# Optimization experiments

Hardware: AMD Instinct MI355X
Metric: run time of the kernel (lower is better)

## Reference

```python
import jax, jax.numpy as jnp
import numpy as np

B, T, C = 32, 2048, 1024  # batch, seq_len (<= block_size), n_embd
HEAD_SIZE = 128


def setup_inputs() -> dict:
    key = jax.random.key(0)
    kx, kk, kq, kv = jax.random.split(key, 4)
    std = 0.02  # CustomLinear init: normal(0, 0.02)
    return {
        "x": jax.random.normal(kx, (B, T, C), dtype=jnp.float32),
        "Wk": jax.random.normal(kk, (HEAD_SIZE, C), dtype=jnp.float32) * std,
        "Wq": jax.random.normal(kq, (HEAD_SIZE, C), dtype=jnp.float32) * std,
        "Wv": jax.random.normal(kv, (HEAD_SIZE, C), dtype=jnp.float32) * std,
    }


def reference(x, Wk, Wq, Wv):
    # x: [B, T, C]; W*: [head_size, C] (torch Linear layout, no bias)
    Bb, Tt, Cc = x.shape
    k = jnp.einsum("btc,hc->bth", x, Wk)
    q = jnp.einsum("btc,hc->bth", x, Wq)
    v = jnp.einsum("btc,hc->bth", x, Wv)
    # NOTE: original scales by C**-0.5 (n_embd), not head_size**-0.5
    wei = jnp.einsum("bth,bsh->bts", q, k) * (Cc ** -0.5)
    causal = jnp.tril(jnp.ones((Tt, Tt), dtype=bool))  # tril[:T,:T]
    wei = jnp.where(causal, wei, -jnp.inf)
    wei = jax.nn.softmax(wei, axis=-1)
    return jnp.einsum("bts,bsh->bth", wei, v)  # [B, T, head_size]
```

## Files before the change

### kernel.cpp

```cpp
#include <hip/hip_runtime.h>
#include <hip/hip_bf16.h>

typedef __bf16 bf8_t __attribute__((ext_vector_type(8)));
typedef __bf16 bf4_t __attribute__((ext_vector_type(4)));
typedef float f4_t __attribute__((ext_vector_type(4)));

#define B_ 32
#define T_ 2048
#define C_ 1024
#define H_ 128

__global__ __launch_bounds__(256, 2) void proj_kernel(
    const float* __restrict__ x,
    const float* __restrict__ Wk, const float* __restrict__ Wq, const float* __restrict__ Wv,
    __bf16* __restrict__ Kb, __bf16* __restrict__ Qb, __bf16* __restrict__ VtG)
{
    __shared__ __bf16 Xs[64][72];
    __shared__ __bf16 Ws[384][72];

    const int m0   = blockIdx.x * 64;
    const int tid  = threadIdx.x;
    const int lane = tid & 63;
    const int wid  = tid >> 6;
    const int lr   = lane & 15;
    const int quad = lane >> 4;

    f4_t acc[3][4][2];
    #pragma unroll
    for (int s = 0; s < 3; s++)
        for (int mi = 0; mi < 4; mi++)
            for (int ni = 0; ni < 2; ni++) acc[s][mi][ni] = f4_t{0.f, 0.f, 0.f, 0.f};

    const int srow = tid >> 4;
    const int sc4  = (tid & 15) << 2;

    float4 xr[4];
    #pragma unroll
    for (int i = 0; i < 4; i++)
        xr[i] = *(const float4*)(x + (size_t)(m0 + srow + i * 16) * C_ + sc4);

    for (int kkI = 0; kkI < 16; kkI++) {
        const int kk = kkI * 64;
        __syncthreads();
        #pragma unroll
        for (int i = 0; i < 4; i++) {
            float4 f = xr[i];
            *(bf4_t*)&Xs[srow + i * 16][sc4] =
                bf4_t{(__bf16)f.x, (__bf16)f.y, (__bf16)f.z, (__bf16)f.w};
        }
        #pragma unroll
        for (int i = 0; i < 24; i++) {
            const int row = srow + i * 16;
            const float* Wp = (row < 128) ? Wk : (row < 256) ? Wq : Wv;
            float4 f = *(const float4*)(Wp + (size_t)(row & 127) * C_ + kk + sc4);
            *(bf4_t*)&Ws[row][sc4] =
                bf4_t{(__bf16)f.x, (__bf16)f.y, (__bf16)f.z, (__bf16)f.w};
        }
        __syncthreads();
        if (kkI < 15) {
            #pragma unroll
            for (int i = 0; i < 4; i++)
                xr[i] = *(const float4*)(x + (size_t)(m0 + srow + i * 16) * C_ + kk + 64 + sc4);
        }
        #pragma unroll
        for (int ks = 0; ks < 2; ks++) {
            const int kb = ks * 32 + quad * 8;
            bf8_t xa[4];
            #pragma unroll
            for (int mi = 0; mi < 4; mi++) xa[mi] = *(const bf8_t*)&Xs[mi * 16 + lr][kb];
            #pragma unroll
            for (int sel = 0; sel < 3; sel++) {
                bf8_t wb[2];
                #pragma unroll
                for (int ni = 0; ni < 2; ni++)
                    wb[ni] = *(const bf8_t*)&Ws[sel * 128 + wid * 32 + ni * 16 + lr][kb];
                if (sel < 2) {
                    #pragma unroll
                    for (int mi = 0; mi < 4; mi++)
                        for (int ni = 0; ni < 2; ni++)
                            acc[sel][mi][ni] = __builtin_amdgcn_mfma_f32_16x16x32_bf16(
                                xa[mi], wb[ni], acc[sel][mi][ni], 0, 0, 0);
                } else {
                    #pragma unroll
                    for (int mi = 0; mi < 4; mi++)
                        for (int ni = 0; ni < 2; ni++)
                            acc[2][mi][ni] = __builtin_amdgcn_mfma_f32_16x16x32_bf16(
                                wb[ni], xa[mi], acc[2][mi][ni], 0, 0, 0);
                }
            }
        }
    }

    #pragma unroll
    for (int sel = 0; sel < 2; sel++) {
        __bf16* Out = (sel == 0) ? Kb : Qb;
        #pragma unroll
        for (int mi = 0; mi < 4; mi++)
            for (int ni = 0; ni < 2; ni++) {
                const int col = wid * 32 + ni * 16 + lr;
                #pragma unroll
                for (int r = 0; r < 4; r++) {
                    const int row = m0 + mi * 16 + quad * 4 + r;
                    Out[(size_t)row * H_ + col] = (__bf16)acc[sel][mi][ni][r];
                }
            }
    }
    {
        const int bb = m0 >> 11;
        const int t0 = m0 & (T_ - 1);
        #pragma unroll
        for (int mi = 0; mi < 4; mi++)
            for (int ni = 0; ni < 2; ni++) {
                const int tok = t0 + mi * 16 + lr;
                #pragma unroll
                for (int r = 0; r < 4; r++) {
                    const int h = wid * 32 + ni * 16 + quad * 4 + r;
                    VtG[(size_t)bb * H_ * T_ + (size_t)h * T_ + tok] = (__bf16)acc[2][mi][ni][r];
                }
            }
    }
}

__global__ __launch_bounds__(512, 4) void flash_kernel(
    const __bf16* __restrict__ Qb, const __bf16* __restrict__ Kb,
    const __bf16* __restrict__ VtG, float* __restrict__ Out)
{
    __shared__ __bf16 Ks[64][136];
    __shared__ __bf16 Vt[128][72];
    __shared__ __bf16 Ps[128][72];

    const int qt = 15 - blockIdx.x;
    const int b  = blockIdx.y;
    const size_t kqbase = (size_t)b * T_ * H_;
    const size_t vbase  = (size_t)b * H_ * T_;

    const int tid  = threadIdx.x;
    const int lane = tid & 63;
    const int w    = tid >> 6;
    const int lr   = lane & 15;
    const int quad = lane >> 4;

    bf8_t qf[4];
    {
        const __bf16* qp = Qb + kqbase + (size_t)(qt * 128 + w * 16 + lr) * H_ + quad * 8;
        #pragma unroll
        for (int ks = 0; ks < 4; ks++) qf[ks] = *(const bf8_t*)(qp + ks * 32);
    }

    f4_t o[8];
    #pragma unroll
    for (int n = 0; n < 8; n++) o[n] = f4_t{0.f, 0.f, 0.f, 0.f};
    float ls[4] = {0.f, 0.f, 0.f, 0.f};

    const float sc = 0.03125f * 1.4426950408889634f;
    const int jmax = 2 * qt + 1;

    for (int j = 0; j <= jmax; j++) {
        __syncthreads();
        #pragma unroll
        for (int i = 0; i < 2; i++) {
            const int u = tid + i * 512, row = u >> 4, c8 = (u & 15) << 3;
            *(bf8_t*)&Ks[row][c8] = *(const bf8_t*)(Kb + kqbase + (size_t)(j * 64 + row) * H_ + c8);
        }
        #pragma unroll
        for (int i = 0; i < 2; i++) {
            const int u = tid + i * 512, h = u >> 3, s8 = (u & 7) << 3;
            *(bf8_t*)&Vt[h][s8] = *(const bf8_t*)(VtG + vbase + (size_t)h * T_ + j * 64 + s8);
        }
        __syncthreads();

        if (j == jmax && w < 4) continue;

        f4_t s4[4];
        #pragma unroll
        for (int n = 0; n < 4; n++) s4[n] = f4_t{0.f, 0.f, 0.f, 0.f};
        #pragma unroll
        for (int ks = 0; ks < 4; ks++)
            for (int n = 0; n < 4; n++) {
                bf8_t kf = *(const bf8_t*)&Ks[n * 16 + lr][ks * 32 + quad * 8];
                s4[n] = __builtin_amdgcn_mfma_f32_16x16x32_bf16(qf[ks], kf, s4[n], 0, 0, 0);
            }

        const bool domask = (j - 2 * qt) == (w >> 2);
        const int rowg = qt * 128 + w * 16 + quad * 4;
        #pragma unroll
        for (int n = 0; n < 4; n++) {
            const int colg = j * 64 + n * 16 + lr;
            #pragma unroll
            for (int r = 0; r < 4; r++) {
                float p = __builtin_exp2f(s4[n][r] * sc);
                if (domask && colg > rowg + r) p = 0.f;
                ls[r] += p;
                Ps[w * 16 + quad * 4 + r][n * 16 + lr] = (__bf16)p;
            }
        }

        #pragma unroll
        for (int ks = 0; ks < 2; ks++) {
            bf8_t pf = *(const bf8_t*)&Ps[w * 16 + lr][ks * 32 + quad * 8];
            #pragma unroll
            for (int n = 0; n < 8; n++) {
                bf8_t vf = *(const bf8_t*)&Vt[n * 16 + lr][ks * 32 + quad * 8];
                o[n] = __builtin_amdgcn_mfma_f32_16x16x32_bf16(pf, vf, o[n], 0, 0, 0);
            }
        }
    }

    float inv[4];
    #pragma unroll
    for (int r = 0; r < 4; r++) {
        float v = ls[r];
        v += __shfl_xor(v, 1);
        v += __shfl_xor(v, 2);
        v += __shfl_xor(v, 4);
        v += __shfl_xor(v, 8);
        inv[r] = 1.f / v;
    }
    #pragma unroll
    for (int n = 0; n < 8; n++) {
        const int col = n * 16 + lr;
        #pragma unroll
        for (int r = 0; r < 4; r++) {
            const int row = qt * 128 + w * 16 + quad * 4 + r;
            Out[kqbase + (size_t)row * H_ + col] = o[n][r] * inv[r];
        }
    }
}

extern "C" void kernel_launch(void* const* d_in, const int* in_sizes, int n_in,
                              void* d_out, int out_size, void* d_ws, size_t ws_size,
                              hipStream_t stream) {
    const float* x  = (const float*)d_in[0];
    const float* Wk = (const float*)d_in[1];
    const float* Wq = (const float*)d_in[2];
    const float* Wv = (const float*)d_in[3];
    float* out = (float*)d_out;

    const size_t n_kqv = (size_t)B_ * T_ * H_;
    __bf16* Kb  = (__bf16*)d_ws;
    __bf16* Qb  = Kb + n_kqv;
    __bf16* VtG = Qb + n_kqv;

    proj_kernel<<<dim3((B_ * T_) / 64), 256, 0, stream>>>(x, Wk, Wq, Wv, Kb, Qb, VtG);
    flash_kernel<<<dim3(16, B_), 512, 0, stream>>>(Qb, Kb, VtG, out);
}
```

Measured before the change: 566.8 us.

## Pre-convert weights to bf16, shrink proj K-tile, prefetch K/V tiles in flash

Adds a small kernel that converts the three weight matrices to bf16 once per call, so the projection kernel loads bf16 weights instead of converting fp32 in every block. The projection uses a 32-wide K step with smaller shared tiles, register prefetch of both X and W, and a reorganised warp-to-column mapping, and raises occupancy to 3 blocks per CU. The flash kernel now prefetches the next K/V tile into registers while computing the current one, and reverses the query-tile order for half the batches to balance the causal workload. The cost is an extra launch and workspace for the bf16 weights, plus more K-loop iterations and syncs in the projection.

```diff
diff --git a/kernel.cpp b/kernel.cpp
--- a/kernel.cpp
+++ b/kernel.cpp
@@ -10,115 +10,123 @@
 #define C_ 1024
 #define H_ 128
 
-__global__ __launch_bounds__(256, 2) void proj_kernel(
-    const float* __restrict__ x,
+__global__ __launch_bounds__(256) void wconv_kernel(
     const float* __restrict__ Wk, const float* __restrict__ Wq, const float* __restrict__ Wv,
+    __bf16* __restrict__ Wb)
+{
+    const int e = (blockIdx.x * 256 + threadIdx.x) * 8;
+    const int arr = e >> 17;
+    const int off = e & 131071;
+    const float* W = (arr == 0) ? Wk : (arr == 1) ? Wq : Wv;
+    float4 f0 = *(const float4*)(W + off);
+    float4 f1 = *(const float4*)(W + off + 4);
+    bf8_t o;
+    o[0] = (__bf16)f0.x; o[1] = (__bf16)f0.y; o[2] = (__bf16)f0.z; o[3] = (__bf16)f0.w;
+    o[4] = (__bf16)f1.x; o[5] = (__bf16)f1.y; o[6] = (__bf16)f1.z; o[7] = (__bf16)f1.w;
+    *(bf8_t*)(Wb + e) = o;
+}
+
+__global__ __launch_bounds__(256, 3) void proj_kernel(
+    const float* __restrict__ x, const __bf16* __restrict__ Wb,
     __bf16* __restrict__ Kb, __bf16* __restrict__ Qb, __bf16* __restrict__ VtG)
 {
-    __shared__ __bf16 Xs[64][72];
-    __shared__ __bf16 Ws[384][72];
+    __shared__ __bf16 Xs[64][40];
+    __shared__ __bf16 Ws[384][40];
 
     const int m0   = blockIdx.x * 64;
     const int tid  = threadIdx.x;
     const int lane = tid & 63;
-    const int wid  = tid >> 6;
+    const int wn   = tid >> 6;
     const int lr   = lane & 15;
     const int quad = lane >> 4;
 
-    f4_t acc[3][4][2];
-    #pragma unroll
-    for (int s = 0; s < 3; s++)
+    f4_t acc[4][6];
+    #pragma unroll
+    for (int mi = 0; mi < 4; mi++)
+        for (int ni = 0; ni < 6; ni++) acc[mi][ni] = f4_t{0.f, 0.f, 0.f, 0.f};
+
+    float4 xr[2];
+    bf8_t  wr[6];
+    #pragma unroll
+    for (int i = 0; i < 2; i++) {
+        const int u = tid + i * 256;
+        xr[i] = *(const float4*)(x + (size_t)(m0 + (u >> 3)) * C_ + ((u & 7) << 2));
+    }
+    #pragma unroll
+    for (int i = 0; i < 6; i++) {
+        const int u = tid + i * 256;
+        wr[i] = *(const bf8_t*)(Wb + (size_t)(u >> 2) * C_ + ((u & 3) << 3));
+    }
+
+    for (int kkI = 0; kkI < 32; kkI++) {
+        __syncthreads();
+        #pragma unroll
+        for (int i = 0; i < 2; i++) {
+            const int u = tid + i * 256;
+            float4 f = xr[i];
+            *(bf4_t*)&Xs[u >> 3][(u & 7) << 2] =
+                bf4_t{(__bf16)f.x, (__bf16)f.y, (__bf16)f.z, (__bf16)f.w};
+        }
+        #pragma unroll
+        for (int i = 0; i < 6; i++) {
+            const int u = tid + i * 256;
+            *(bf8_t*)&Ws[u >> 2][(u & 3) << 3] = wr[i];
+        }
+        __syncthreads();
+        if (kkI < 31) {
+            const int kk = (kkI + 1) * 32;
+            #pragma unroll
+            for (int i = 0; i < 2; i++) {
+                const int u = tid + i * 256;
+                xr[i] = *(const float4*)(x + (size_t)(m0 + (u >> 3)) * C_ + kk + ((u & 7) << 2));
+            }
+            #pragma unroll
+            for (int i = 0; i < 6; i++) {
+                const int u = tid + i * 256;
+                wr[i] = *(const bf8_t*)(Wb + (size_t)(u >> 2) * C_ + kk + ((u & 3) << 3));
+            }
+        }
+        bf8_t xa[4];
+        #pragma unroll
+        for (int mi = 0; mi < 4; mi++) xa[mi] = *(const bf8_t*)&Xs[mi * 16 + lr][quad * 8];
+        #pragma unroll
+        for (int ni = 0; ni < 6; ni++) {
+            bf8_t wb = *(const bf8_t*)&Ws[ni * 64 + wn * 16 + lr][quad * 8];
+            if (ni < 4) {
+                #pragma unroll
+                for (int mi = 0; mi < 4; mi++)
+                    acc[mi][ni] = __builtin_amdgcn_mfma_f32_16x16x32_bf16(xa[mi], wb, acc[mi][ni], 0, 0, 0);
+            } else {
+                #pragma unroll
+                for (int mi = 0; mi < 4; mi++)
+                    acc[mi][ni] = __builtin_amdgcn_mfma_f32_16x16x32_bf16(wb, xa[mi], acc[mi][ni], 0, 0, 0);
+            }
+        }
+    }
+
+    const int bb = m0 >> 11;
+    const int t0 = m0 & (T_ - 1);
+    #pragma unroll
+    for (int ni = 0; ni < 4; ni++) {
+        __bf16* Out = (ni < 2) ? Kb : Qb;
+        const int col = (ni & 1) * 64 + wn * 16 + lr;
+        #pragma unroll
         for (int mi = 0; mi < 4; mi++)
-            for (int ni = 0; ni < 2; ni++) acc[s][mi][ni] = f4_t{0.f, 0.f, 0.f, 0.f};
-
-    const int srow = tid >> 4;
-    const int sc4  = (tid & 15) << 2;
-
-    float4 xr[4];
-    #pragma unroll
-    for (int i = 0; i < 4; i++)
-        xr[i] = *(const float4*)(x + (size_t)(m0 + srow + i * 16) * C_ + sc4);
-
-    for (int kkI = 0; kkI < 16; kkI++) {
-        const int kk = kkI * 64;
-        __syncthreads();
-        #pragma unroll
-        for (int i = 0; i < 4; i++) {
-            float4 f = xr[i];
-            *(bf4_t*)&Xs[srow + i * 16][sc4] =
-                bf4_t{(__bf16)f.x, (__bf16)f.y, (__bf16)f.z, (__bf16)f.w};
-        }
-        #pragma unroll
-        for (int i = 0; i < 24; i++) {
-            const int row = srow + i * 16;
-            const float* Wp = (row < 128) ? Wk : (row < 256) ? Wq : Wv;
-            float4 f = *(const float4*)(Wp + (size_t)(row & 127) * C_ + kk + sc4);
-            *(bf4_t*)&Ws[row][sc4] =
-                bf4_t{(__bf16)f.x, (__bf16)f.y, (__bf16)f.z, (__bf16)f.w};
-        }
-        __syncthreads();
-        if (kkI < 15) {
-            #pragma unroll
-            for (int i = 0; i < 4; i++)
-                xr[i] = *(const float4*)(x + (size_t)(m0 + srow + i * 16) * C_ + kk + 64 + sc4);
-        }
-        #pragma unroll
-        for (int ks = 0; ks < 2; ks++) {
-            const int kb = ks * 32 + quad * 8;
-            bf8_t xa[4];
-            #pragma unroll
-            for (int mi = 0; mi < 4; mi++) xa[mi] = *(const bf8_t*)&Xs[mi * 16 + lr][kb];
-            #pragma unroll
-            for (int sel = 0; sel < 3; sel++) {
-                bf8_t wb[2];
-                #pragma unroll
-                for (int ni = 0; ni < 2; ni++)
-                    wb[ni] = *(const bf8_t*)&Ws[sel * 128 + wid * 32 + ni * 16 + lr][kb];
-                if (sel < 2) {
-                    #pragma unroll
-                    for (int mi = 0; mi < 4; mi++)
-                        for (int ni = 0; ni < 2; ni++)
-                            acc[sel][mi][ni] = __builtin_amdgcn_mfma_f32_16x16x32_bf16(
-                                xa[mi], wb[ni], acc[sel][mi][ni], 0, 0, 0);
-                } else {
-                    #pragma unroll
-                    for (int mi = 0; mi < 4; mi++)
-                        for (int ni = 0; ni < 2; ni++)
-                            acc[2][mi][ni] = __builtin_amdgcn_mfma_f32_16x16x32_bf16(
-                                wb[ni], xa[mi], acc[2][mi][ni], 0, 0, 0);
-                }
-            }
-        }
-    }
-
-    #pragma unroll
-    for (int sel = 0; sel < 2; sel++) {
-        __bf16* Out = (sel == 0) ? Kb : Qb;
-        #pragma unroll
-        for (int mi = 0; mi < 4; mi++)
-            for (int ni = 0; ni < 2; ni++) {
-                const int col = wid * 32 + ni * 16 + lr;
-                #pragma unroll
-                for (int r = 0; r < 4; r++) {
-                    const int row = m0 + mi * 16 + quad * 4 + r;
-                    Out[(size_t)row * H_ + col] = (__bf16)acc[sel][mi][ni][r];
-                }
-            }
-    }
-    {
-        const int bb = m0 >> 11;
-        const int t0 = m0 & (T_ - 1);
-        #pragma unroll
-        for (int mi = 0; mi < 4; mi++)
-            for (int ni = 0; ni < 2; ni++) {
-                const int tok = t0 + mi * 16 + lr;
-                #pragma unroll
-                for (int r = 0; r < 4; r++) {
-                    const int h = wid * 32 + ni * 16 + quad * 4 + r;
-                    VtG[(size_t)bb * H_ * T_ + (size_t)h * T_ + tok] = (__bf16)acc[2][mi][ni][r];
-                }
-            }
-    }
+            for (int r = 0; r < 4; r++) {
+                const int row = m0 + mi * 16 + quad * 4 + r;
+                Out[(size_t)row * H_ + col] = (__bf16)acc[mi][ni][r];
+            }
+    }
+    #pragma unroll
+    for (int ni = 4; ni < 6; ni++)
+        for (int mi = 0; mi < 4; mi++) {
+            const int tok = t0 + mi * 16 + lr;
+            #pragma unroll
+            for (int r = 0; r < 4; r++) {
+                const int h = (ni - 4) * 64 + wn * 16 + quad * 4 + r;
+                VtG[(size_t)bb * H_ * T_ + (size_t)h * T_ + tok] = (__bf16)acc[mi][ni][r];
+            }
+        }
 }
 
 __global__ __launch_bounds__(512, 4) void flash_kernel(
@@ -129,7 +137,7 @@
     __shared__ __bf16 Vt[128][72];
     __shared__ __bf16 Ps[128][72];
 
-    const int qt = 15 - blockIdx.x;
+    const int qt = (blockIdx.y < 16) ? (15 - blockIdx.x) : blockIdx.x;
     const int b  = blockIdx.y;
     const size_t kqbase = (size_t)b * T_ * H_;
     const size_t vbase  = (size_t)b * H_ * T_;
@@ -155,20 +163,30 @@
     const float sc = 0.03125f * 1.4426950408889634f;
     const int jmax = 2 * qt + 1;
 
+    const int kRow0 = tid >> 4,          kC0 = (tid & 15) << 3;
+    const int kRow1 = (tid + 512) >> 4,  kC1 = ((tid + 512) & 15) << 3;
+    const int vH0 = tid >> 3,            vS0 = (tid & 7) << 3;
+    const int vH1 = (tid + 512) >> 3,    vS1 = ((tid + 512) & 7) << 3;
+
+    bf8_t kr0 = *(const bf8_t*)(Kb + kqbase + (size_t)kRow0 * H_ + kC0);
+    bf8_t kr1 = *(const bf8_t*)(Kb + kqbase + (size_t)kRow1 * H_ + kC1);
+    bf8_t vr0 = *(const bf8_t*)(VtG + vbase + (size_t)vH0 * T_ + vS0);
+    bf8_t vr1 = *(const bf8_t*)(VtG + vbase + (size_t)vH1 * T_ + vS1);
+
     for (int j = 0; j <= jmax; j++) {
         __syncthreads();
-        #pragma unroll
-        for (int i = 0; i < 2; i++) {
-            const int u = tid + i * 512, row = u >> 4, c8 = (u & 15) << 3;
-            *(bf8_t*)&Ks[row][c8] = *(const bf8_t*)(Kb + kqbase + (size_t)(j * 64 + row) * H_ + c8);
-        }
-        #pragma unroll
-        for (int i = 0; i < 2; i++) {
-            const int u = tid + i * 512, h = u >> 3, s8 = (u & 7) << 3;
-            *(bf8_t*)&Vt[h][s8] = *(const bf8_t*)(VtG + vbase + (size_t)h * T_ + j * 64 + s8);
-        }
-        __syncthreads();
-
+        *(bf8_t*)&Ks[kRow0][kC0] = kr0;
+        *(bf8_t*)&Ks[kRow1][kC1] = kr1;
+        *(bf8_t*)&Vt[vH0][vS0]   = vr0;
+        *(bf8_t*)&Vt[vH1][vS1]   = vr1;
+        __syncthreads();
+        if (j < jmax) {
+            const int s0 = (j + 1) * 64;
+            kr0 = *(const bf8_t*)(Kb + kqbase + (size_t)(s0 + kRow0) * H_ + kC0);
+            kr1 = *(const bf8_t*)(Kb + kqbase + (size_t)(s0 + kRow1) * H_ + kC1);
+            vr0 = *(const bf8_t*)(VtG + vbase + (size_t)vH0 * T_ + s0 + vS0);
+            vr1 = *(const bf8_t*)(VtG + vbase + (size_t)vH1 * T_ + s0 + vS1);
+        }
         if (j == jmax && w < 4) continue;
 
         f4_t s4[4];
@@ -240,7 +258,9 @@
     __bf16* Kb  = (__bf16*)d_ws;
     __bf16* Qb  = Kb + n_kqv;
     __bf16* VtG = Qb + n_kqv;
-
-    proj_kernel<<<dim3((B_ * T_) / 64), 256, 0, stream>>>(x, Wk, Wq, Wv, Kb, Qb, VtG);
+    __bf16* Wb  = VtG + n_kqv;
+
+    wconv_kernel<<<dim3(192), 256, 0, stream>>>(Wk, Wq, Wv, Wb);
+    proj_kernel<<<dim3((B_ * T_) / 64), 256, 0, stream>>>(x, Wb, Kb, Qb, VtG);
     flash_kernel<<<dim3(16, B_), 512, 0, stream>>>(Qb, Kb, VtG, out);
 }
```

New measurement: 510.2 us. 1.11x faster.
